# Optimization experiments

Measured on AMD Instinct MI355X. Metric: run time of the kernel, lower is better.

## Reference

```python
import jax, jax.numpy as jnp
import numpy as np

HEADS = 12
SPLIT = 4


def setup_inputs() -> dict:
    key = jax.random.key(0)
    ks = jax.random.split(key, 4)
    B, N, C = 4, 4096, 768
    C1 = C // 2
    x = jax.random.normal(ks[0], (B, N, C), dtype=jnp.float32)
    W_reduce = jax.random.normal(ks[1], (C, C1), dtype=jnp.float32) * (C ** -0.5)
    b_reduce = jnp.zeros((C1,), dtype=jnp.float32)
    W_qkv = jax.random.normal(ks[2], (C1, 3 * C1), dtype=jnp.float32) * (C1 ** -0.5)
    b_qkv = jnp.zeros((3 * C1,), dtype=jnp.float32)
    W_proj = jax.random.normal(ks[3], (C1, C), dtype=jnp.float32) * (C1 ** -0.5)
    b_proj = jnp.zeros((C,), dtype=jnp.float32)
    return {"x": x, "W_reduce": W_reduce, "b_reduce": b_reduce,
            "W_qkv": W_qkv, "b_qkv": b_qkv, "W_proj": W_proj, "b_proj": b_proj}


def reference(x, W_reduce, b_reduce, W_qkv, b_qkv, W_proj, b_proj):
    B, N, C = x.shape
    C1 = C // 2
    H = HEADS
    hd = C1 // H
    seg = N // SPLIT
    # reduce: (B,N,C) -> (B,N,C1)
    xr = x @ W_reduce + b_reduce
    # qkv: (B,N,3,H,hd)
    qkv = (xr @ W_qkv + b_qkv).reshape(B, N, 3, H, hd)
    q, k, v = qkv[:, :, 0], qkv[:, :, 1], qkv[:, :, 2]  # (B,N,H,hd)
    # to (B,H,split,seg,hd) for block-local attention
    def blk(t):
        return t.transpose(0, 2, 1, 3).reshape(B, H, SPLIT, seg, hd)
    qb, kb, vb = blk(q), blk(k), blk(v)
    scale = hd ** -0.5
    scores = jnp.einsum('bhsqd,bhskd->bhsqk', qb, kb) * scale  # (B,H,split,seg,seg)
    attn = jax.nn.softmax(scores, axis=-1)
    ob = jnp.einsum('bhsqk,bhskd->bhsqd', attn, vb)  # (B,H,split,seg,hd)
    # concat over split (dim 2 of (B,H,N,hd)), permute -> (B,N,C1)
    o = ob.transpose(0, 2, 3, 1, 4).reshape(B, N, C1)
    return o @ W_proj + b_proj
```

## Files before the change

### kernel.cpp

```cpp
#include <hip/hip_runtime.h>
#include <hip/hip_bf16.h>

typedef __attribute__((ext_vector_type(8))) short   s16x8;
typedef __attribute__((ext_vector_type(4))) short   s16x4;
typedef __attribute__((ext_vector_type(8))) __bf16  bf16x8;
typedef __attribute__((ext_vector_type(4))) float   f32x4;

__device__ __forceinline__ short f2bf(float f) {
  unsigned u = __builtin_bit_cast(unsigned, f);
  u += 0x7fffu + ((u >> 16) & 1u);
  return (short)(u >> 16);
}

__device__ __forceinline__ unsigned cvt2bf(float a, float b) {
  __hip_bfloat162 r = __float22bfloat162_rn(make_float2(a, b));
  unsigned u;
  __builtin_memcpy(&u, &r, 4);
  return u;
}

__device__ __forceinline__ f32x4 mfma16(s16x8 a, s16x8 b, f32x4 c) {
  return __builtin_amdgcn_mfma_f32_16x16x32_bf16(
      __builtin_bit_cast(bf16x8, a), __builtin_bit_cast(bf16x8, b), c, 0, 0, 0);
}

__device__ __forceinline__ void glds16(const short* g, short* l) {
  __builtin_amdgcn_global_load_lds(
      (__attribute__((address_space(1))) const void*)g,
      (__attribute__((address_space(3))) void*)l, 16, 0, 0);
}

__global__ __launch_bounds__(256) void transpose_cast_all(
    const float* __restrict__ s0, short* __restrict__ d0,
    const float* __restrict__ s1, short* __restrict__ d1,
    const float* __restrict__ s2, short* __restrict__ d2) {
  __shared__ float t[32 * 33];
  int id = blockIdx.x;
  const float* src; short* dst; int R, C, bx, by;
  if (id < 288)      { src = s0; dst = d0; R = 768; C = 384;  bx = id % 12;           by = id / 12; }
  else if (id < 720) { int l = id - 288; src = s1; dst = d1; R = 384; C = 1152; bx = l % 36; by = l / 36; }
  else               { int l = id - 720; src = s2; dst = d2; R = 384; C = 768;  bx = l % 24; by = l / 24; }
  int tid = threadIdx.x;
  int c0 = bx * 32, r0 = by * 32;
  for (int rep = 0; rep < 4; ++rep) {
    int idx = rep * 256 + tid;
    int rr = idx >> 5, cc = idx & 31;
    t[rr * 33 + cc] = src[(size_t)(r0 + rr) * C + c0 + cc];
  }
  __syncthreads();
  for (int rep = 0; rep < 4; ++rep) {
    int idx = rep * 256 + tid;
    int cc = idx >> 5, rr = idx & 31;
    dst[(size_t)(c0 + cc) * R + r0 + rr] = f2bf(t[rr * 33 + cc]);
  }
}

template <int MODE, bool AF32, int BM>
__global__ __launch_bounds__(256, 2) void gemm_bf16(
    const short* __restrict__ A, const float* __restrict__ Af,
    const short* __restrict__ Bt,
    const float* __restrict__ bias, void* __restrict__ out,
    short* __restrict__ q_p, short* __restrict__ k_p, short* __restrict__ vt,
    int M, int N, int K) {
  constexpr int WM  = BM / 2;
  constexpr int MI  = WM / 16;
  constexpr int AIT = BM / 32;
  __shared__ short lds[2][(BM + 128) * 64];
  int tid = threadIdx.x;
  int lane = tid & 63, wid = tid >> 6;
  int l15 = lane & 15, g = lane >> 4;
  int nbn = N >> 7;
  int nwg = gridDim.x;
  int bid = blockIdx.x;
  int chunk = nwg >> 3;
  int swz_bid = (bid & 7) * chunk + (bid >> 3);
  int bm = swz_bid / nbn, bn = swz_bid % nbn;
  int wr = wid >> 1, wc = wid & 1;

  const short* Ab = AF32 ? nullptr : (A + (size_t)(bm * BM) * K);
  const float* Afb = AF32 ? (Af + (size_t)(bm * BM) * K) : nullptr;
  const short* Bb = Bt + (size_t)(bn * 128) * K;

  f32x4 acc[MI][4];
#pragma unroll
  for (int i = 0; i < MI; ++i)
#pragma unroll
    for (int j = 0; j < 4; ++j) acc[i][j] = (f32x4){0.f, 0.f, 0.f, 0.f};

  f32x4 areg[AIT][2];
  int nk = K >> 6;

  auto stageB = [&](int bufi, int kt) {
    const short* gb = Bb + kt * 64;
#pragma unroll
    for (int it = 0; it < 4; ++it) {
      int c = it * 256 + tid;
      int row = c >> 3, pc = c & 7;
      int lc = pc ^ (row & 7);
      glds16(gb + (size_t)row * K + lc * 8,
             &lds[bufi][BM * 64 + (it * 256 + wid * 64) * 8]);
    }
  };
  auto stageA_lds = [&](int bufi, int kt) {
    const short* ga = Ab + kt * 64;
#pragma unroll
    for (int it = 0; it < AIT; ++it) {
      int c = it * 256 + tid;
      int row = c >> 3, pc = c & 7;
      int lc = pc ^ (row & 7);
      glds16(ga + (size_t)row * K + lc * 8,
             &lds[bufi][(it * 256 + wid * 64) * 8]);
    }
  };
  auto stageA_issue = [&](int kt) {
#pragma unroll
    for (int it = 0; it < AIT; ++it) {
      int c = it * 256 + tid;
      int row = c >> 3, pc = c & 7;
      int lc = pc ^ (row & 7);
      const float* src = Afb + (size_t)row * K + kt * 64 + lc * 8;
      areg[it][0] = *(const f32x4*)(src);
      areg[it][1] = *(const f32x4*)(src + 4);
    }
  };
  auto stageA_write = [&](int bufi) {
#pragma unroll
    for (int it = 0; it < AIT; ++it) {
      int c = it * 256 + tid;
      s16x8 o;
#pragma unroll
      for (int q = 0; q < 4; ++q) {
        o[q]     = f2bf(areg[it][0][q]);
        o[q + 4] = f2bf(areg[it][1][q]);
      }
      *(s16x8*)(&lds[bufi][0] + (size_t)c * 8) = o;
    }
  };

  if (AF32) { stageA_issue(0); stageB(0, 0); stageA_write(0); }
  else      { stageA_lds(0, 0); stageB(0, 0); }
  __syncthreads();
  int buf = 0;
  for (int kt = 0; kt < nk; ++kt) {
    bool more = (kt + 1 < nk);
    if (more) {
      if (AF32) stageA_issue(kt + 1); else stageA_lds(buf ^ 1, kt + 1);
      stageB(buf ^ 1, kt + 1);
    }
    const short* la = &lds[buf][0];
    const short* lb = &lds[buf][BM * 64];
    s16x8 af[MI][2], bfv[4][2];
#pragma unroll
    for (int i = 0; i < MI; ++i)
#pragma unroll
      for (int kk = 0; kk < 2; ++kk) {
        int row = wr * WM + i * 16 + l15;
        int ch = (kk * 4 + g) ^ (l15 & 7);
        af[i][kk] = *(const s16x8*)(la + row * 64 + ch * 8);
      }
#pragma unroll
    for (int j = 0; j < 4; ++j)
#pragma unroll
      for (int kk = 0; kk < 2; ++kk) {
        int row = wc * 64 + j * 16 + l15;
        int ch = (kk * 4 + g) ^ (l15 & 7);
        bfv[j][kk] = *(const s16x8*)(lb + row * 64 + ch * 8);
      }
#pragma unroll
    for (int kk = 0; kk < 2; ++kk)
#pragma unroll
      for (int i = 0; i < MI; ++i)
#pragma unroll
        for (int j = 0; j < 4; ++j)
          acc[i][j] = mfma16(af[i][kk], bfv[j][kk], acc[i][j]);
    if (AF32 && more) stageA_write(buf ^ 1);
    __syncthreads();
    buf ^= 1;
  }

#pragma unroll
  for (int j = 0; j < 4; ++j) {
    int col = bn * 128 + wc * 64 + j * 16 + l15;
    float bv = bias[col];
    int which = 0, rem = 0, h = 0, d = 0;
    if (MODE == 2) {
      which = col / 384;
      rem = col - which * 384;
      h = rem >> 5; d = rem & 31;
    }
#pragma unroll
    for (int i = 0; i < MI; ++i) {
      int row0 = bm * BM + wr * WM + i * 16 + g * 4;
      if (MODE == 2 && which == 2) {
        int b = row0 >> 12, s = (row0 >> 10) & 3, key = row0 & 1023;
        s16x4 o;
#pragma unroll
        for (int r = 0; r < 4; ++r) o[r] = f2bf(acc[i][j][r] + bv);
        *(s16x4*)(vt + ((size_t)((b * 12 + h) * 4 + s) << 15) + d * 1024 + key) = o;
        continue;
      }
#pragma unroll
      for (int r = 0; r < 4; ++r) {
        int row = row0 + r;
        float v = acc[i][j][r] + bv;
        if (MODE == 1) {
          ((float*)out)[(size_t)row * N + col] = v;
        } else if (MODE == 0) {
          ((short*)out)[(size_t)row * N + col] = f2bf(v);
        } else {
          if (which == 0) v *= (0.17677669529663687f * 1.4426950408889634f);
          short bf = f2bf(v);
          int b = row >> 12, s = (row >> 10) & 3, key = row & 1023;
          size_t dst = ((size_t)((b * 12 + h) * 4 + s) << 15) + key * 32 + d;
          if (which) k_p[dst] = bf; else q_p[dst] = bf;
        }
      }
    }
  }
}

__global__ __launch_bounds__(128, 2) void attn_kernel(
    const short* __restrict__ qp, const short* __restrict__ kp,
    const short* __restrict__ vt, short* __restrict__ ob) {
  __shared__ short plds[2][32 * 136];
  int tid = threadIdx.x;
  int lane = tid & 63, w = tid >> 6;
  int l15 = lane & 15, g = lane >> 4;
  int bid = blockIdx.x;
  int bhs = bid % 192, qt = bid / 192;
  int s = bhs & 3, h = (bhs >> 2) % 12, b = bhs / 48;

  const short* qb = qp + ((size_t)bhs << 15) + (qt * 64 + w * 32) * 32;
  const short* kb = kp + ((size_t)bhs << 15);
  const short* vb = vt + ((size_t)bhs << 15);

  s16x8 qf[2];
#pragma unroll
  for (int i = 0; i < 2; ++i)
    qf[i] = *(const s16x8*)(qb + (i * 16 + l15) * 32 + g * 8);

  f32x4 oacc[2][2];
#pragma unroll
  for (int i = 0; i < 2; ++i)
#pragma unroll
    for (int n = 0; n < 2; ++n) oacc[i][n] = (f32x4){0.f, 0.f, 0.f, 0.f};
  float lsum[2] = {0.f, 0.f};

  char* pw = (char*)&plds[w][0];
  int swz = (l15 >> 3) << 4;

  for (int t = 0; t < 8; ++t) {
    f32x4 sa[2][8];
#pragma unroll
    for (int i = 0; i < 2; ++i)
#pragma unroll
      for (int kn = 0; kn < 8; ++kn) sa[i][kn] = (f32x4){0.f, 0.f, 0.f, 0.f};
#pragma unroll
    for (int kn = 0; kn < 8; ++kn) {
      s16x8 kf = *(const s16x8*)(kb + (size_t)(t * 128 + kn * 16 + l15) * 32 + g * 8);
      sa[0][kn] = mfma16(kf, qf[0], sa[0][kn]);
      sa[1][kn] = mfma16(kf, qf[1], sa[1][kn]);
    }
#pragma unroll
    for (int i = 0; i < 2; ++i) {
      float ps = 0.f;
#pragma unroll
      for (int kn = 0; kn < 8; ++kn) {
        float p0 = __builtin_amdgcn_exp2f(sa[i][kn][0]);
        float p1 = __builtin_amdgcn_exp2f(sa[i][kn][1]);
        float p2 = __builtin_amdgcn_exp2f(sa[i][kn][2]);
        float p3 = __builtin_amdgcn_exp2f(sa[i][kn][3]);
        ps += (p0 + p1) + (p2 + p3);
        uint2 u;
        u.x = cvt2bf(p0, p1);
        u.y = cvt2bf(p2, p3);
        *(s16x4*)(pw + (i * 16 + l15) * 272 + ((kn * 32 + g * 8) ^ swz)) =
            __builtin_bit_cast(s16x4, u);
      }
      lsum[i] += ps;
    }
    __builtin_amdgcn_sched_barrier(0x7F);
#pragma unroll
    for (int kk = 0; kk < 4; ++kk) {
      s16x8 pa[2];
#pragma unroll
      for (int i = 0; i < 2; ++i)
        pa[i] = *(const s16x8*)(pw + (i * 16 + l15) * 272 + ((kk * 64 + g * 16) ^ swz));
#pragma unroll
      for (int n = 0; n < 2; ++n) {
        s16x8 vf = *(const s16x8*)(vb + (size_t)(n * 16 + l15) * 1024 + t * 128 + kk * 32 + g * 8);
        oacc[0][n] = mfma16(vf, pa[0], oacc[0][n]);
        oacc[1][n] = mfma16(vf, pa[1], oacc[1][n]);
      }
    }
    __builtin_amdgcn_sched_barrier(0x7F);
  }
#pragma unroll
  for (int i = 0; i < 2; ++i) {
    float v = lsum[i];
    v += __shfl_xor(v, 16);
    v += __shfl_xor(v, 32);
    lsum[i] = v;
  }
  int tokq0 = b * 4096 + s * 1024 + qt * 64 + w * 32;
#pragma unroll
  for (int i = 0; i < 2; ++i) {
    float inv = 1.0f / lsum[i];
    int tok = tokq0 + i * 16 + l15;
#pragma unroll
    for (int n = 0; n < 2; ++n) {
      uint2 u;
      u.x = cvt2bf(oacc[i][n][0] * inv, oacc[i][n][1] * inv);
      u.y = cvt2bf(oacc[i][n][2] * inv, oacc[i][n][3] * inv);
      *(s16x4*)(ob + (size_t)tok * 384 + h * 32 + n * 16 + g * 4) =
          __builtin_bit_cast(s16x4, u);
    }
  }
}

extern "C" void kernel_launch(void* const* d_in, const int* in_sizes, int n_in,
                              void* d_out, int out_size, void* d_ws, size_t ws_size,
                              hipStream_t stream) {
  const float* x        = (const float*)d_in[0];
  const float* W_reduce = (const float*)d_in[1];
  const float* b_reduce = (const float*)d_in[2];
  const float* W_qkv    = (const float*)d_in[3];
  const float* b_qkv    = (const float*)d_in[4];
  const float* W_proj   = (const float*)d_in[5];
  const float* b_proj   = (const float*)d_in[6];
  float* out = (float*)d_out;

  char* ws = (char*)d_ws;
  short* wr_t    = (short*)(ws + 0);
  short* wqkv_t  = (short*)(ws + 589824);
  short* wproj_t = (short*)(ws + 1474560);
  short* xr_b    = (short*)(ws + 2064384);
  short* o_b     = xr_b;
  short* q_p     = (short*)(ws + 14647296);
  short* k_p     = (short*)(ws + 27230208);
  short* vt      = (short*)(ws + 39813120);

  transpose_cast_all<<<1008, 256, 0, stream>>>(W_reduce, wr_t, W_qkv, wqkv_t, W_proj, wproj_t);

  gemm_bf16<0, true, 64><<<768, 256, 0, stream>>>(nullptr, x, wr_t, b_reduce, xr_b,
                                                  nullptr, nullptr, nullptr, 16384, 384, 768);
  gemm_bf16<2, false, 64><<<2304, 256, 0, stream>>>(xr_b, nullptr, wqkv_t, b_qkv, nullptr,
                                                    q_p, k_p, vt, 16384, 1152, 384);
  attn_kernel<<<3072, 128, 0, stream>>>(q_p, k_p, vt, o_b);
  gemm_bf16<1, false, 64><<<1536, 256, 0, stream>>>(o_b, nullptr, wproj_t, b_proj, (void*)out,
                                                    nullptr, nullptr, nullptr, 16384, 768, 384);
}
```

Baseline: 138.1 us.

## Use 32x32x16 MFMA in attention and pass P via cross-lane shuffles instead of LDS

The attention kernel switches from 16x16x32 MFMA tiles to 32x32x16 tiles, so each wave computes a 32-query by 32-key score block with two MFMAs. Instead of writing exp-probabilities to shared memory and reading them back as A operands, the bf16 P fragments are rearranged in registers with xor-32 lane shuffles and fed straight into the PV MFMA. This removes the LDS round trip, the swizzle arithmetic and the scheduling barriers. In exchange it adds shuffle and select instructions, and the K/V loads become smaller per-iteration chunks that may be less latency-hidden.

```diff
diff --git a/kernel.cpp b/kernel.cpp
--- a/kernel.cpp
+++ b/kernel.cpp
@@ -1,10 +1,12 @@
 #include <hip/hip_runtime.h>
 #include <hip/hip_bf16.h>
 
-typedef __attribute__((ext_vector_type(8))) short   s16x8;
-typedef __attribute__((ext_vector_type(4))) short   s16x4;
-typedef __attribute__((ext_vector_type(8))) __bf16  bf16x8;
-typedef __attribute__((ext_vector_type(4))) float   f32x4;
+typedef __attribute__((ext_vector_type(8)))  short    s16x8;
+typedef __attribute__((ext_vector_type(4)))  short    s16x4;
+typedef __attribute__((ext_vector_type(8)))  __bf16   bf16x8;
+typedef __attribute__((ext_vector_type(4)))  float    f32x4;
+typedef __attribute__((ext_vector_type(16))) float    f32x16;
+typedef __attribute__((ext_vector_type(4)))  unsigned u32x4;
 
 __device__ __forceinline__ short f2bf(float f) {
   unsigned u = __builtin_bit_cast(unsigned, f);
@@ -21,6 +23,11 @@
 
 __device__ __forceinline__ f32x4 mfma16(s16x8 a, s16x8 b, f32x4 c) {
   return __builtin_amdgcn_mfma_f32_16x16x32_bf16(
+      __builtin_bit_cast(bf16x8, a), __builtin_bit_cast(bf16x8, b), c, 0, 0, 0);
+}
+
+__device__ __forceinline__ f32x16 mfma32(s16x8 a, s16x8 b, f32x16 c) {
+  return __builtin_amdgcn_mfma_f32_32x32x16_bf16(
       __builtin_bit_cast(bf16x8, a), __builtin_bit_cast(bf16x8, b), c, 0, 0, 0);
 }
 
@@ -222,99 +229,74 @@
 __global__ __launch_bounds__(128, 2) void attn_kernel(
     const short* __restrict__ qp, const short* __restrict__ kp,
     const short* __restrict__ vt, short* __restrict__ ob) {
-  __shared__ short plds[2][32 * 136];
   int tid = threadIdx.x;
   int lane = tid & 63, w = tid >> 6;
-  int l15 = lane & 15, g = lane >> 4;
+  int l31 = lane & 31, hh = lane >> 5;
   int bid = blockIdx.x;
   int bhs = bid % 192, qt = bid / 192;
   int s = bhs & 3, h = (bhs >> 2) % 12, b = bhs / 48;
 
-  const short* qb = qp + ((size_t)bhs << 15) + (qt * 64 + w * 32) * 32;
+  int q0 = qt * 64 + w * 32;
+  const short* qb = qp + ((size_t)bhs << 15) + q0 * 32;
   const short* kb = kp + ((size_t)bhs << 15);
   const short* vb = vt + ((size_t)bhs << 15);
 
   s16x8 qf[2];
-#pragma unroll
-  for (int i = 0; i < 2; ++i)
-    qf[i] = *(const s16x8*)(qb + (i * 16 + l15) * 32 + g * 8);
-
-  f32x4 oacc[2][2];
-#pragma unroll
-  for (int i = 0; i < 2; ++i)
-#pragma unroll
-    for (int n = 0; n < 2; ++n) oacc[i][n] = (f32x4){0.f, 0.f, 0.f, 0.f};
-  float lsum[2] = {0.f, 0.f};
-
-  char* pw = (char*)&plds[w][0];
-  int swz = (l15 >> 3) << 4;
+  qf[0] = *(const s16x8*)(qb + l31 * 32 + hh * 8);
+  qf[1] = *(const s16x8*)(qb + l31 * 32 + 16 + hh * 8);
+
+  f32x16 oacc;
+#pragma unroll
+  for (int r = 0; r < 16; ++r) oacc[r] = 0.f;
+  float lsum = 0.f;
 
   for (int t = 0; t < 8; ++t) {
-    f32x4 sa[2][8];
-#pragma unroll
-    for (int i = 0; i < 2; ++i)
-#pragma unroll
-      for (int kn = 0; kn < 8; ++kn) sa[i][kn] = (f32x4){0.f, 0.f, 0.f, 0.f};
-#pragma unroll
-    for (int kn = 0; kn < 8; ++kn) {
-      s16x8 kf = *(const s16x8*)(kb + (size_t)(t * 128 + kn * 16 + l15) * 32 + g * 8);
-      sa[0][kn] = mfma16(kf, qf[0], sa[0][kn]);
-      sa[1][kn] = mfma16(kf, qf[1], sa[1][kn]);
-    }
-#pragma unroll
-    for (int i = 0; i < 2; ++i) {
+#pragma unroll
+    for (int kb32 = 0; kb32 < 4; ++kb32) {
+      int keybase = t * 128 + kb32 * 32;
+      const short* kaddr = kb + (size_t)(keybase + l31) * 32 + hh * 8;
+      s16x8 kf0 = *(const s16x8*)(kaddr);
+      s16x8 kf1 = *(const s16x8*)(kaddr + 16);
+      f32x16 sa;
+#pragma unroll
+      for (int r = 0; r < 16; ++r) sa[r] = 0.f;
+      sa = mfma32(kf0, qf[0], sa);
+      sa = mfma32(kf1, qf[1], sa);
+      float p[16];
       float ps = 0.f;
 #pragma unroll
-      for (int kn = 0; kn < 8; ++kn) {
-        float p0 = __builtin_amdgcn_exp2f(sa[i][kn][0]);
-        float p1 = __builtin_amdgcn_exp2f(sa[i][kn][1]);
-        float p2 = __builtin_amdgcn_exp2f(sa[i][kn][2]);
-        float p3 = __builtin_amdgcn_exp2f(sa[i][kn][3]);
-        ps += (p0 + p1) + (p2 + p3);
-        uint2 u;
-        u.x = cvt2bf(p0, p1);
-        u.y = cvt2bf(p2, p3);
-        *(s16x4*)(pw + (i * 16 + l15) * 272 + ((kn * 32 + g * 8) ^ swz)) =
-            __builtin_bit_cast(s16x4, u);
-      }
-      lsum[i] += ps;
-    }
-    __builtin_amdgcn_sched_barrier(0x7F);
-#pragma unroll
-    for (int kk = 0; kk < 4; ++kk) {
-      s16x8 pa[2];
-#pragma unroll
-      for (int i = 0; i < 2; ++i)
-        pa[i] = *(const s16x8*)(pw + (i * 16 + l15) * 272 + ((kk * 64 + g * 16) ^ swz));
-#pragma unroll
-      for (int n = 0; n < 2; ++n) {
-        s16x8 vf = *(const s16x8*)(vb + (size_t)(n * 16 + l15) * 1024 + t * 128 + kk * 32 + g * 8);
-        oacc[0][n] = mfma16(vf, pa[0], oacc[0][n]);
-        oacc[1][n] = mfma16(vf, pa[1], oacc[1][n]);
-      }
-    }
-    __builtin_amdgcn_sched_barrier(0x7F);
-  }
-#pragma unroll
-  for (int i = 0; i < 2; ++i) {
-    float v = lsum[i];
-    v += __shfl_xor(v, 16);
-    v += __shfl_xor(v, 32);
-    lsum[i] = v;
-  }
-  int tokq0 = b * 4096 + s * 1024 + qt * 64 + w * 32;
-#pragma unroll
-  for (int i = 0; i < 2; ++i) {
-    float inv = 1.0f / lsum[i];
-    int tok = tokq0 + i * 16 + l15;
-#pragma unroll
-    for (int n = 0; n < 2; ++n) {
-      uint2 u;
-      u.x = cvt2bf(oacc[i][n][0] * inv, oacc[i][n][1] * inv);
-      u.y = cvt2bf(oacc[i][n][2] * inv, oacc[i][n][3] * inv);
-      *(s16x4*)(ob + (size_t)tok * 384 + h * 32 + n * 16 + g * 4) =
-          __builtin_bit_cast(s16x4, u);
-    }
+      for (int r = 0; r < 16; ++r) {
+        p[r] = __builtin_amdgcn_exp2f(sa[r]);
+        ps += p[r];
+      }
+      lsum += ps;
+      unsigned u[8];
+#pragma unroll
+      for (int j = 0; j < 8; ++j) u[j] = cvt2bf(p[2 * j], p[2 * j + 1]);
+      unsigned y0 = __shfl_xor(hh ? u[0] : u[2], 32);
+      unsigned y1 = __shfl_xor(hh ? u[1] : u[3], 32);
+      unsigned y2 = __shfl_xor(hh ? u[4] : u[6], 32);
+      unsigned y3 = __shfl_xor(hh ? u[5] : u[7], 32);
+      u32x4 f0 = { hh ? y0 : u[0], hh ? y1 : u[1], hh ? u[2] : y0, hh ? u[3] : y1 };
+      u32x4 f1 = { hh ? y2 : u[4], hh ? y3 : u[5], hh ? u[6] : y2, hh ? u[7] : y3 };
+      const short* vaddr = vb + (size_t)l31 * 1024 + keybase + hh * 8;
+      s16x8 vf0 = *(const s16x8*)(vaddr);
+      s16x8 vf1 = *(const s16x8*)(vaddr + 16);
+      oacc = mfma32(vf0, __builtin_bit_cast(s16x8, f0), oacc);
+      oacc = mfma32(vf1, __builtin_bit_cast(s16x8, f1), oacc);
+    }
+  }
+  lsum += __shfl_xor(lsum, 32);
+  float inv = 1.0f / lsum;
+  int tok = b * 4096 + s * 1024 + q0 + l31;
+  short* obase = ob + (size_t)tok * 384 + h * 32;
+#pragma unroll
+  for (int rg = 0; rg < 4; ++rg) {
+    int d = 8 * rg + 4 * hh;
+    uint2 uo;
+    uo.x = cvt2bf(oacc[rg * 4 + 0] * inv, oacc[rg * 4 + 1] * inv);
+    uo.y = cvt2bf(oacc[rg * 4 + 2] * inv, oacc[rg * 4 + 3] * inv);
+    *(s16x4*)(obase + d) = __builtin_bit_cast(s16x4, uo);
   }
 }
 
```

Result: slower. 144.8 us (+4.8%).
